# Kernel optimization log

Hardware: AMD Instinct MI355X
Metric: run time of the kernel (lower is better)

## Reference

```python
import jax, jax.numpy as jnp
import numpy as np

B, N, IN_NF, EDGE_NF = 2, 512, 3, 1
DIM, HEADS, DHEAD, DEPTH = 256, 8, 32, 2
INNER = HEADS * DHEAD
SCALE = DHEAD ** -0.5


def _layernorm(x, g, b):
    m = jnp.mean(x, axis=-1, keepdims=True)
    v = jnp.mean((x - m) ** 2, axis=-1, keepdims=True)
    return (x - m) / jnp.sqrt(v + 1e-5) * g + b


def _rotate_half(x):
    x1, x2 = jnp.split(x, 2, axis=-1)
    return jnp.concatenate([-x2, x1], axis=-1)


def _rotary_freqs(n):
    inv_freq = 1.0 / (10000.0 ** (jnp.arange(0, DHEAD, 2, dtype=jnp.float32) / DHEAD))
    f = jnp.einsum('i,j->ij', jnp.arange(n, dtype=jnp.float32), inv_freq)
    return jnp.concatenate([f, f], axis=-1)  # [n, DHEAD]


def _apply_rotary(freqs, t):
    return t * jnp.cos(freqs) + _rotate_half(t) * jnp.sin(freqs)


def _cdist(x):
    # pairwise L2 distances with grad-safe sqrt at zero (matches torch.cdist fwd)
    d2 = jnp.sum((x[:, :, None, :] - x[:, None, :, :]) ** 2, axis=-1)
    safe = jnp.where(d2 > 0.0, d2, 1.0)
    return jnp.where(d2 > 0.0, jnp.sqrt(safe), 0.0)


def setup_inputs():
    key = jax.random.key(0)
    ks = jax.random.split(key, 12)
    w = lambda k, *shape: jax.random.normal(k, shape, dtype=jnp.float32) * 0.02
    return dict(
        x=jax.random.normal(ks[0], (B, N, IN_NF), dtype=jnp.float32),
        t=jax.random.uniform(ks[1], (B, N, 1), dtype=jnp.float32),
        W_enc=w(ks[2], IN_NF + 1, DIM),
        W_dec=w(ks[3], DIM, IN_NF),
        ln_g=jnp.ones((DEPTH, DIM), jnp.float32),
        ln_b=jnp.zeros((DEPTH, DIM), jnp.float32),
        Wq=w(ks[4], DEPTH, DIM, INNER),
        bq=jnp.zeros((DEPTH, INNER), jnp.float32),
        Wkv=w(ks[5], DEPTH, DIM, 2 * INNER),
        bkv=jnp.zeros((DEPTH, 2 * INNER), jnp.float32),
        We=w(ks[6], DEPTH, EDGE_NF, INNER),
        be=jnp.zeros((DEPTH, INNER), jnp.float32),
        Wo=w(ks[7], DEPTH, INNER, DIM),
        bo=jnp.zeros((DEPTH, DIM), jnp.float32),
        Wg=w(ks[8], DEPTH, 3 * DIM, 1),
    )


def _forward(x, t, W_enc, W_dec, ln_g, ln_b, Wq, bq, Wkv, bkv, We, be, Wo, bo, Wg):
    b, n, _ = x.shape
    edges = _cdist(x)[..., None]                         # [B,N,N,1]
    nodes = jnp.concatenate([x, t], axis=-1) @ W_enc     # [B,N,DIM]
    freqs = _rotary_freqs(n)
    for l in range(DEPTH):
        h = _layernorm(nodes, ln_g[l], ln_b[l])          # PreNorm
        q = (h @ Wq[l] + bq[l]).reshape(b, n, HEADS, DHEAD).transpose(0, 2, 1, 3)
        k, v = jnp.split(h @ Wkv[l] + bkv[l], 2, axis=-1)
        k = k.reshape(b, n, HEADS, DHEAD).transpose(0, 2, 1, 3)
        v = v.reshape(b, n, HEADS, DHEAD).transpose(0, 2, 1, 3)
        e = (edges @ We[l] + be[l]).reshape(b, n, n, HEADS, DHEAD)  # [B,i,j,H,D]
        q = _apply_rotary(freqs, q)
        k = _apply_rotary(freqs, k)
        # sim = q . (k_j + e_ij); split to avoid an extra [B,H,N,N,D] materialization
        sim = (jnp.einsum('bhid,bhjd->bhij', q, k)
               + jnp.einsum('bhid,bijhd->bhij', q, e)) * SCALE
        attn = jax.nn.softmax(sim, axis=-1)
        # out = attn . (v_j + e_ij)
        out = (jnp.einsum('bhij,bhjd->bhid', attn, v)
               + jnp.einsum('bhij,bijhd->bhid', attn, e))
        out = out.transpose(0, 2, 1, 3).reshape(b, n, INNER) @ Wo[l] + bo[l]
        # gated residual
        gate = jax.nn.sigmoid(
            jnp.concatenate([out, nodes, out - nodes], axis=-1) @ Wg[l])
        nodes = out * gate + nodes * (1.0 - gate)
    return nodes @ W_dec                                  # [B,N,IN_NF]


def reference(x, t, W_enc, W_dec, ln_g, ln_b, Wq, bq, Wkv, bkv, We, be, Wo, bo, Wg):
    return _forward(x, t, W_enc, W_dec, ln_g, ln_b, Wq, bq, Wkv, bkv, We, be, Wo, bo, Wg)
```

## Files before the change

### kernel.cpp

```cpp
#include <hip/hip_runtime.h>
#include <math.h>

#define B 2
#define N 512
#define DIM 256
#define HEADS 8
#define DHEAD 32
#define INNER 256
#define DEPTH 2
#define SCALE 0.17677669529663687f

__device__ __forceinline__ float block_sum256(float v, float* red4) {
    #pragma unroll
    for (int o = 32; o; o >>= 1) v += __shfl_xor(v, o);
    int tid = threadIdx.x;
    __syncthreads();
    if ((tid & 63) == 0) red4[tid >> 6] = v;
    __syncthreads();
    return red4[0] + red4[1] + red4[2] + red4[3];
}

__global__ void k_pre(const float* __restrict__ x, const float* __restrict__ t,
                      const float* __restrict__ Wenc,
                      const float* __restrict__ ln_g, const float* __restrict__ ln_b,
                      float* __restrict__ nodes, float* __restrict__ hbuf,
                      float* __restrict__ dist,
                      float* __restrict__ ct, float* __restrict__ st) {
    __shared__ float red4[4];
    __shared__ float xs[N * 3];
    int row = blockIdx.x, d = threadIdx.x;
    int b = row >> 9, i = row & (N - 1);

    if (d < 8) {
        int idx = blockIdx.x * 8 + d;
        int ii = idx >> 4, jj = idx & 15;
        float invf = powf(10000.0f, -(float)jj / 16.0f);
        float ang = (float)ii * invf;
        ct[idx] = cosf(ang);
        st[idx] = sinf(ang);
    }

    float x0 = x[row*3+0], x1 = x[row*3+1], x2 = x[row*3+2], tt = t[row];
    float nv = x0*Wenc[d] + x1*Wenc[DIM+d] + x2*Wenc[2*DIM+d] + tt*Wenc[3*DIM+d];
    nodes[row*DIM + d] = nv;
    float mean = block_sum256(nv, red4) * (1.0f/DIM);
    float c = nv - mean;
    float var = block_sum256(c*c, red4) * (1.0f/DIM);
    hbuf[row*DIM + d] = c * (1.0f/sqrtf(var + 1e-5f)) * ln_g[d] + ln_b[d];

    for (int f = d; f < N*3; f += 256) xs[f] = x[b*N*3 + f];
    __syncthreads();
    float xi0 = xs[i*3+0], xi1 = xs[i*3+1], xi2 = xs[i*3+2];
    for (int j = d; j < N; j += 256) {
        float d0 = xi0 - xs[j*3+0], d1 = xi1 - xs[j*3+1], d2 = xi2 - xs[j*3+2];
        float s = d0*d0 + d1*d1 + d2*d2;
        dist[(size_t)row*N + j] = (s > 0.f) ? sqrtf(s) : 0.f;
    }
}

__global__ __launch_bounds__(256, 4)
void k_gemm_qkv(const float* __restrict__ hbuf,
                const float* __restrict__ Wq, const float* __restrict__ bq,
                const float* __restrict__ Wkv, const float* __restrict__ bkv,
                const float* __restrict__ We, const float* __restrict__ be,
                const float* __restrict__ ct, const float* __restrict__ st,
                float* __restrict__ qbuf, float* __restrict__ kbuf, float* __restrict__ vbuf,
                float* __restrict__ qwe, float* __restrict__ qbe, int layer) {
    __shared__ float AT[64][32];
    __shared__ float Bs[64][64];

    int tid = threadIdx.x;
    int mt = blockIdx.x & 31;
    int nt = blockIdx.x >> 5;
    int tx = tid & 15, ty = tid >> 4;
    int n0 = nt * 64;

    const float* Wsrc; int wstride;
    if (n0 < 256) { Wsrc = Wq  + (size_t)layer*256*256 + n0;        wstride = 256; }
    else          { Wsrc = Wkv + (size_t)layer*256*512 + (n0-256);  wstride = 512; }

    float acc[2][4] = {{0,0,0,0},{0,0,0,0}};

    int am = tid & 31, ak = tid >> 5;
    int bn4 = tid & 15, bk = tid >> 4;

    for (int kt = 0; kt < 4; ++kt) {
        int kbase = kt * 64;
        if (kt) __syncthreads();
        {
            const float* src = hbuf + (size_t)(mt*32 + am)*256 + kbase + ak*8;
            float4 a0 = *(const float4*)src;
            float4 a1 = *(const float4*)(src + 4);
            AT[ak*8+0][am]=a0.x; AT[ak*8+1][am]=a0.y; AT[ak*8+2][am]=a0.z; AT[ak*8+3][am]=a0.w;
            AT[ak*8+4][am]=a1.x; AT[ak*8+5][am]=a1.y; AT[ak*8+6][am]=a1.z; AT[ak*8+7][am]=a1.w;
        }
        #pragma unroll
        for (int p = 0; p < 4; ++p) {
            int k = bk + p*16;
            float4 v = *(const float4*)(Wsrc + (size_t)(kbase + k)*wstride + bn4*4);
            *(float4*)&Bs[k][bn4*4] = v;
        }
        __syncthreads();
        #pragma unroll 8
        for (int k = 0; k < 64; ++k) {
            float2 a = *(const float2*)&AT[k][ty*2];
            float4 b = *(const float4*)&Bs[k][tx*4];
            acc[0][0] += a.x*b.x; acc[0][1] += a.x*b.y; acc[0][2] += a.x*b.z; acc[0][3] += a.x*b.w;
            acc[1][0] += a.y*b.x; acc[1][1] += a.y*b.y; acc[1][2] += a.y*b.z; acc[1][3] += a.y*b.w;
        }
    }

    int row = mt*32 + ty*2;
    int n = n0 + tx*4;

    float4 bias4;
    if (n0 < 256) bias4 = *(const float4*)&bq[layer*256 + n];
    else          bias4 = *(const float4*)&bkv[layer*512 + (n - 256)];
    #pragma unroll
    for (int r = 0; r < 2; ++r) {
        acc[r][0] += bias4.x; acc[r][1] += bias4.y; acc[r][2] += bias4.z; acc[r][3] += bias4.w;
    }

    if (n0 >= 512) {
        #pragma unroll
        for (int r = 0; r < 2; ++r) {
            float4 o = make_float4(acc[r][0], acc[r][1], acc[r][2], acc[r][3]);
            *(float4*)&vbuf[(size_t)(row + r)*256 + (n - 512)] = o;
        }
        return;
    }

    float* sh = &Bs[0][0];
    __syncthreads();
    #pragma unroll
    for (int r = 0; r < 2; ++r)
        #pragma unroll
        for (int c = 0; c < 4; ++c)
            sh[(ty*2 + r)*68 + tx*4 + c] = acc[r][c];
    __syncthreads();

    float wep[2] = {0.f, 0.f}, bep[2] = {0.f, 0.f};
    float val[2][4];
    #pragma unroll
    for (int r = 0; r < 2; ++r) {
        int ii = (row + r) & (N-1);
        #pragma unroll
        for (int c = 0; c < 4; ++c) {
            int tc = tx*4 + c;
            int dd = tc & 31, jj = tc & 15;
            float ca = ct[ii*16 + jj], sa = st[ii*16 + jj];
            int ptc = (dd < 16) ? tc + 16 : tc - 16;
            float sgn = (dd < 16) ? -1.f : 1.f;
            float partner = sh[(ty*2 + r)*68 + ptc];
            float rot = acc[r][c]*ca + sgn*partner*sa;
            val[r][c] = rot;
            if (n0 < 256) {
                wep[r] += rot * We[layer*256 + n0 + tc];
                bep[r] += rot * be[layer*256 + n0 + tc];
            }
        }
    }

    float* dst = (n0 < 256) ? qbuf : kbuf;
    int coln = (n0 < 256) ? n : n - 256;
    #pragma unroll
    for (int r = 0; r < 2; ++r) {
        float4 o = make_float4(val[r][0], val[r][1], val[r][2], val[r][3]);
        *(float4*)&dst[(size_t)(row + r)*256 + coln] = o;
    }

    if (n0 < 256) {
        #pragma unroll
        for (int r = 0; r < 2; ++r) {
            wep[r] += __shfl_xor(wep[r], 1); bep[r] += __shfl_xor(bep[r], 1);
            wep[r] += __shfl_xor(wep[r], 2); bep[r] += __shfl_xor(bep[r], 2);
            wep[r] += __shfl_xor(wep[r], 4); bep[r] += __shfl_xor(bep[r], 4);
        }
        if ((tid & 7) == 0) {
            int h = nt*2 + (tx >> 3);
            int bb = row >> 9;
            #pragma unroll
            for (int r = 0; r < 2; ++r) {
                int ii = (row + r) & (N-1);
                qwe[(bb*HEADS + h)*N + ii] = wep[r];
                qbe[(bb*HEADS + h)*N + ii] = bep[r];
            }
        }
    }
}

#define TI 16
__global__ __launch_bounds__(256, 2)
void k_attn(const float* __restrict__ qbuf, const float* __restrict__ kbuf,
            const float* __restrict__ vbuf,
            const float* __restrict__ qwe, const float* __restrict__ qbe,
            const float* __restrict__ dist,
            const float* __restrict__ We, const float* __restrict__ be,
            float* __restrict__ attnout, int layer) {
    __shared__ float Tt[32 * 128];

    int t = threadIdx.x;
    int g = t & 31;
    int r = t >> 5;
    int bid = blockIdx.x;
    int itile = bid & 31;
    int h = (bid >> 5) & (HEADS-1);
    int b = bid >> 8;
    int i0 = itile * TI + r;
    int i1 = i0 + 8;

    int scol = t & 127;
    int d0   = (t >> 7) * 16;

    float q0[32], q1[32];
    {
        const float4* qp0 = (const float4*)(qbuf + (size_t)(b*N + i0) * INNER + h * DHEAD);
        const float4* qp1 = (const float4*)(qbuf + (size_t)(b*N + i1) * INNER + h * DHEAD);
        #pragma unroll
        for (int c = 0; c < 8; ++c) {
            float4 v0 = qp0[c], v1 = qp1[c];
            q0[c*4+0] = v0.x; q0[c*4+1] = v0.y; q0[c*4+2] = v0.z; q0[c*4+3] = v0.w;
            q1[c*4+0] = v1.x; q1[c*4+1] = v1.y; q1[c*4+2] = v1.z; q1[c*4+3] = v1.w;
        }
    }
    float qw0 = qwe[(b*HEADS + h)*N + i0], qb0 = qbe[(b*HEADS + h)*N + i0];
    float qw1 = qwe[(b*HEADS + h)*N + i1], qb1 = qbe[(b*HEADS + h)*N + i1];

    const float* kbase = kbuf + (size_t)b*N*INNER + h*DHEAD;
    const float* vbase = vbuf + (size_t)b*N*INNER + h*DHEAD;
    const float* drow0 = dist + (size_t)(b*N + i0) * N;
    const float* drow1 = dist + (size_t)(b*N + i1) * N;

    float sim0[16], sim1[16];

    #pragma unroll
    for (int jt = 0; jt < 4; ++jt) {
        if (jt) __syncthreads();
        {
            const float* src = kbase + (size_t)(jt*128 + scol) * INNER + d0;
            float4 a0 = *(const float4*)(src + 0);
            float4 a1 = *(const float4*)(src + 4);
            float4 a2 = *(const float4*)(src + 8);
            float4 a3 = *(const float4*)(src + 12);
            Tt[(d0+ 0)*128 + scol] = a0.x; Tt[(d0+ 1)*128 + scol] = a0.y;
            Tt[(d0+ 2)*128 + scol] = a0.z; Tt[(d0+ 3)*128 + scol] = a0.w;
            Tt[(d0+ 4)*128 + scol] = a1.x; Tt[(d0+ 5)*128 + scol] = a1.y;
            Tt[(d0+ 6)*128 + scol] = a1.z; Tt[(d0+ 7)*128 + scol] = a1.w;
            Tt[(d0+ 8)*128 + scol] = a2.x; Tt[(d0+ 9)*128 + scol] = a2.y;
            Tt[(d0+10)*128 + scol] = a2.z; Tt[(d0+11)*128 + scol] = a2.w;
            Tt[(d0+12)*128 + scol] = a3.x; Tt[(d0+13)*128 + scol] = a3.y;
            Tt[(d0+14)*128 + scol] = a3.z; Tt[(d0+15)*128 + scol] = a3.w;
        }
        __syncthreads();
        float4 s0 = make_float4(0.f,0.f,0.f,0.f);
        float4 s1 = make_float4(0.f,0.f,0.f,0.f);
        #pragma unroll
        for (int d = 0; d < 32; ++d) {
            float4 kv = *(const float4*)&Tt[d*128 + g*4];
            float qa = q0[d], qc = q1[d];
            s0.x += qa*kv.x; s0.y += qa*kv.y; s0.z += qa*kv.z; s0.w += qa*kv.w;
            s1.x += qc*kv.x; s1.y += qc*kv.y; s1.z += qc*kv.z; s1.w += qc*kv.w;
        }
        float4 dv0 = *(const float4*)&drow0[jt*128 + g*4];
        float4 dv1 = *(const float4*)&drow1[jt*128 + g*4];
        sim0[jt*4+0] = (s0.x + dv0.x*qw0 + qb0) * SCALE;
        sim0[jt*4+1] = (s0.y + dv0.y*qw0 + qb0) * SCALE;
        sim0[jt*4+2] = (s0.z + dv0.z*qw0 + qb0) * SCALE;
        sim0[jt*4+3] = (s0.w + dv0.w*qw0 + qb0) * SCALE;
        sim1[jt*4+0] = (s1.x + dv1.x*qw1 + qb1) * SCALE;
        sim1[jt*4+1] = (s1.y + dv1.y*qw1 + qb1) * SCALE;
        sim1[jt*4+2] = (s1.z + dv1.z*qw1 + qb1) * SCALE;
        sim1[jt*4+3] = (s1.w + dv1.w*qw1 + qb1) * SCALE;
    }

    float mx0 = -1e30f, mx1 = -1e30f;
    #pragma unroll
    for (int v = 0; v < 16; ++v) { mx0 = fmaxf(mx0, sim0[v]); mx1 = fmaxf(mx1, sim1[v]); }
    #pragma unroll
    for (int o = 1; o <= 16; o <<= 1) {
        mx0 = fmaxf(mx0, __shfl_xor(mx0, o));
        mx1 = fmaxf(mx1, __shfl_xor(mx1, o));
    }

    float ls0 = 0.f, ld0 = 0.f, ls1 = 0.f, ld1 = 0.f;
    #pragma unroll
    for (int jt = 0; jt < 4; ++jt) {
        float4 dv0 = *(const float4*)&drow0[jt*128 + g*4];
        float4 dv1 = *(const float4*)&drow1[jt*128 + g*4];
        float a0[4] = {dv0.x,dv0.y,dv0.z,dv0.w};
        float a1[4] = {dv1.x,dv1.y,dv1.z,dv1.w};
        #pragma unroll
        for (int u = 0; u < 4; ++u) {
            float p0 = __expf(sim0[jt*4+u] - mx0);
            float p1 = __expf(sim1[jt*4+u] - mx1);
            sim0[jt*4+u] = p0; sim1[jt*4+u] = p1;
            ls0 += p0; ld0 += p0 * a0[u];
            ls1 += p1; ld1 += p1 * a1[u];
        }
    }
    #pragma unroll
    for (int o = 1; o <= 16; o <<= 1) {
        ls0 += __shfl_xor(ls0, o); ld0 += __shfl_xor(ld0, o);
        ls1 += __shfl_xor(ls1, o); ld1 += __shfl_xor(ld1, o);
    }

    float acc0[32], acc1[32];
    #pragma unroll
    for (int d = 0; d < 32; ++d) { acc0[d] = 0.f; acc1[d] = 0.f; }

    #pragma unroll
    for (int jt = 0; jt < 4; ++jt) {
        __syncthreads();
        {
            const float* src = vbase + (size_t)(jt*128 + scol) * INNER + d0;
            float4 a0 = *(const float4*)(src + 0);
            float4 a1 = *(const float4*)(src + 4);
            float4 a2 = *(const float4*)(src + 8);
            float4 a3 = *(const float4*)(src + 12);
            Tt[(d0+ 0)*128 + scol] = a0.x; Tt[(d0+ 1)*128 + scol] = a0.y;
            Tt[(d0+ 2)*128 + scol] = a0.z; Tt[(d0+ 3)*128 + scol] = a0.w;
            Tt[(d0+ 4)*128 + scol] = a1.x; Tt[(d0+ 5)*128 + scol] = a1.y;
            Tt[(d0+ 6)*128 + scol] = a1.z; Tt[(d0+ 7)*128 + scol] = a1.w;
            Tt[(d0+ 8)*128 + scol] = a2.x; Tt[(d0+ 9)*128 + scol] = a2.y;
            Tt[(d0+10)*128 + scol] = a2.z; Tt[(d0+11)*128 + scol] = a2.w;
            Tt[(d0+12)*128 + scol] = a3.x; Tt[(d0+13)*128 + scol] = a3.y;
            Tt[(d0+14)*128 + scol] = a3.z; Tt[(d0+15)*128 + scol] = a3.w;
        }
        __syncthreads();
        float p00 = sim0[jt*4+0], p01 = sim0[jt*4+1], p02 = sim0[jt*4+2], p03 = sim0[jt*4+3];
        float p10 = sim1[jt*4+0], p11 = sim1[jt*4+1], p12 = sim1[jt*4+2], p13 = sim1[jt*4+3];
        #pragma unroll
        for (int d = 0; d < 32; ++d) {
            float4 vv = *(const float4*)&Tt[d*128 + g*4];
            acc0[d] += p00*vv.x + p01*vv.y + p02*vv.z + p03*vv.w;
            acc1[d] += p10*vv.x + p11*vv.y + p12*vv.z + p13*vv.w;
        }
    }

    #pragma unroll
    for (int d = 0; d < 32; ++d) {
        #pragma unroll
        for (int o = 1; o <= 16; o <<= 1) {
            acc0[d] += __shfl_xor(acc0[d], o);
            acc1[d] += __shfl_xor(acc1[d], o);
        }
    }

    float il0 = 1.0f / ls0, il1 = 1.0f / ls1;
    float ad0 = ld0 * il0, ad1 = ld1 * il1;
    float o0 = acc0[0], o1 = acc1[0];
    #pragma unroll
    for (int d = 1; d < 32; ++d) if (g == d) { o0 = acc0[d]; o1 = acc1[d]; }
    float wv = We[layer*INNER + h*DHEAD + g];
    float bv = be[layer*INNER + h*DHEAD + g];
    attnout[(size_t)(b*N + i0)*INNER + h*DHEAD + g] = o0*il0 + ad0*wv + bv;
    attnout[(size_t)(b*N + i1)*INNER + h*DHEAD + g] = o1*il1 + ad1*wv + bv;
}

__global__ __launch_bounds__(256, 4)
void k_gemm_o(const float* __restrict__ attnout, const float* __restrict__ Wo,
              const float* __restrict__ bo, float* __restrict__ obuf, int layer) {
    __shared__ float AT[64][32];
    __shared__ float Bs[64][32];
    int tid = threadIdx.x;
    int mt = blockIdx.x & 31, nt = blockIdx.x >> 5;
    int tx = tid & 7, ty = tid >> 3;

    float acc[4] = {0,0,0,0};
    int am = tid & 31, ak = tid >> 5;
    int bn4 = tid & 7, bk = tid >> 3;
    const float* Wsrc = Wo + (size_t)layer*256*256 + nt*32;

    for (int kt = 0; kt < 4; ++kt) {
        int kbase = kt * 64;
        if (kt) __syncthreads();
        {
            const float* src = attnout + (size_t)(mt*32 + am)*256 + kbase + ak*8;
            float4 a0 = *(const float4*)src;
            float4 a1 = *(const float4*)(src + 4);
            AT[ak*8+0][am]=a0.x; AT[ak*8+1][am]=a0.y; AT[ak*8+2][am]=a0.z; AT[ak*8+3][am]=a0.w;
            AT[ak*8+4][am]=a1.x; AT[ak*8+5][am]=a1.y; AT[ak*8+6][am]=a1.z; AT[ak*8+7][am]=a1.w;
        }
        #pragma unroll
        for (int p = 0; p < 2; ++p) {
            int k = bk + p*32;
            *(float4*)&Bs[k][bn4*4] = *(const float4*)(Wsrc + (size_t)(kbase + k)*256 + bn4*4);
        }
        __syncthreads();
        #pragma unroll 8
        for (int k = 0; k < 64; ++k) {
            float a = AT[k][ty];
            float4 b = *(const float4*)&Bs[k][tx*4];
            acc[0] += a*b.x; acc[1] += a*b.y; acc[2] += a*b.z; acc[3] += a*b.w;
        }
    }
    int row = mt*32 + ty, n = nt*32 + tx*4;
    float4 bias = *(const float4*)&bo[layer*256 + n];
    float4 o = make_float4(acc[0]+bias.x, acc[1]+bias.y, acc[2]+bias.z, acc[3]+bias.w);
    *(float4*)&obuf[(size_t)row*256 + n] = o;
}

__global__ void k_gate_ln(const float* __restrict__ obuf, const float* __restrict__ Wg,
                          const float* __restrict__ ln_g, const float* __restrict__ ln_b,
                          const float* __restrict__ Wdec,
                          float* __restrict__ nodes, float* __restrict__ hbuf,
                          float* __restrict__ out, int layer) {
    __shared__ float red4[4];
    int row = blockIdx.x, d = threadIdx.x;
    float o  = obuf[row*DIM + d];
    float nd = nodes[row*DIM + d];
    const float* Wgl = Wg + layer*3*DIM;
    float s = o*Wgl[d] + nd*Wgl[DIM+d] + (o-nd)*Wgl[2*DIM+d];
    float tot = block_sum256(s, red4);
    float gate = 1.0f/(1.0f + __expf(-tot));
    float nn = o*gate + nd*(1.0f - gate);
    nodes[row*DIM + d] = nn;
    if (layer == 0) {
        float mean = block_sum256(nn, red4) * (1.0f/DIM);
        float c = nn - mean;
        float var = block_sum256(c*c, red4) * (1.0f/DIM);
        hbuf[row*DIM + d] = c * (1.0f/sqrtf(var + 1e-5f)) * ln_g[DIM + d] + ln_b[DIM + d];
    } else {
        float s0 = block_sum256(nn * Wdec[d*3+0], red4);
        float s1 = block_sum256(nn * Wdec[d*3+1], red4);
        float s2 = block_sum256(nn * Wdec[d*3+2], red4);
        if (d == 0) { out[row*3+0] = s0; out[row*3+1] = s1; out[row*3+2] = s2; }
    }
}

extern "C" void kernel_launch(void* const* d_in, const int* in_sizes, int n_in,
                              void* d_out, int out_size, void* d_ws, size_t ws_size,
                              hipStream_t stream) {
    const float* x     = (const float*)d_in[0];
    const float* t     = (const float*)d_in[1];
    const float* W_enc = (const float*)d_in[2];
    const float* W_dec = (const float*)d_in[3];
    const float* ln_g  = (const float*)d_in[4];
    const float* ln_b  = (const float*)d_in[5];
    const float* Wq    = (const float*)d_in[6];
    const float* bq    = (const float*)d_in[7];
    const float* Wkv   = (const float*)d_in[8];
    const float* bkv   = (const float*)d_in[9];
    const float* We    = (const float*)d_in[10];
    const float* be    = (const float*)d_in[11];
    const float* Wo    = (const float*)d_in[12];
    const float* bo    = (const float*)d_in[13];
    const float* Wg    = (const float*)d_in[14];
    float* out = (float*)d_out;

    float* ws = (float*)d_ws;
    float* nodes   = ws;
    float* dist    = nodes   + B*N*DIM;
    float* hbuf    = dist    + B*N*N;
    float* qbuf    = hbuf    + B*N*DIM;
    float* kbuf    = qbuf    + B*N*INNER;
    float* vbuf    = kbuf    + B*N*INNER;
    float* qwe     = vbuf    + B*N*INNER;
    float* qbe     = qwe     + B*HEADS*N;
    float* attnout = qbe     + B*HEADS*N;
    float* obuf    = attnout + B*N*INNER;
    float* ct      = obuf    + B*N*DIM;
    float* st      = ct      + N*16;

    k_pre<<<B*N, DIM, 0, stream>>>(x, t, W_enc, ln_g, ln_b, nodes, hbuf, dist, ct, st);
    for (int l = 0; l < DEPTH; ++l) {
        k_gemm_qkv<<<384, 256, 0, stream>>>(hbuf, Wq, bq, Wkv, bkv, We, be, ct, st,
                                            qbuf, kbuf, vbuf, qwe, qbe, l);
        k_attn<<<B*HEADS*(N/TI), 256, 0, stream>>>(qbuf, kbuf, vbuf, qwe, qbe, dist, We, be,
                                                   attnout, l);
        k_gemm_o<<<256, 256, 0, stream>>>(attnout, Wo, bo, obuf, l);
        k_gate_ln<<<B*N, DIM, 0, stream>>>(obuf, Wg, ln_g, ln_b, W_dec, nodes, hbuf, out, l);
    }
}
```

Before: 113.3 us.

## Fuse encoder/gate/layernorm into QKV GEMM and recompute distances inside attention

Removes the separate pre-processing and gate/layernorm kernels. The encoder, or the previous layer's gated residual plus layernorm, is now computed per 32-row tile inside the QKV GEMM prologue and kept in shared memory. Pairwise distances are recomputed from coordinates held in shared memory inside attention instead of being read from a materialized N×N buffer. Rotary sin/cos are also computed inline instead of looked up from tables. This cuts two launches and global traffic, at the cost of every column-tile block repeating the layernorm and gate work. Attention also does extra sqrt work.

```diff
diff --git a/kernel.cpp b/kernel.cpp
--- a/kernel.cpp
+++ b/kernel.cpp
@@ -9,6 +9,7 @@
 #define INNER 256
 #define DEPTH 2
 #define SCALE 0.17677669529663687f
+#define L2INVF 0.8304820237218406f
 
 __device__ __forceinline__ float block_sum256(float v, float* red4) {
     #pragma unroll
@@ -20,93 +21,107 @@
     return red4[0] + red4[1] + red4[2] + red4[3];
 }
 
-__global__ void k_pre(const float* __restrict__ x, const float* __restrict__ t,
-                      const float* __restrict__ Wenc,
-                      const float* __restrict__ ln_g, const float* __restrict__ ln_b,
-                      float* __restrict__ nodes, float* __restrict__ hbuf,
-                      float* __restrict__ dist,
-                      float* __restrict__ ct, float* __restrict__ st) {
-    __shared__ float red4[4];
-    __shared__ float xs[N * 3];
-    int row = blockIdx.x, d = threadIdx.x;
-    int b = row >> 9, i = row & (N - 1);
-
-    if (d < 8) {
-        int idx = blockIdx.x * 8 + d;
-        int ii = idx >> 4, jj = idx & 15;
-        float invf = powf(10000.0f, -(float)jj / 16.0f);
-        float ang = (float)ii * invf;
-        ct[idx] = cosf(ang);
-        st[idx] = sinf(ang);
-    }
-
-    float x0 = x[row*3+0], x1 = x[row*3+1], x2 = x[row*3+2], tt = t[row];
-    float nv = x0*Wenc[d] + x1*Wenc[DIM+d] + x2*Wenc[2*DIM+d] + tt*Wenc[3*DIM+d];
-    nodes[row*DIM + d] = nv;
-    float mean = block_sum256(nv, red4) * (1.0f/DIM);
-    float c = nv - mean;
-    float var = block_sum256(c*c, red4) * (1.0f/DIM);
-    hbuf[row*DIM + d] = c * (1.0f/sqrtf(var + 1e-5f)) * ln_g[d] + ln_b[d];
-
-    for (int f = d; f < N*3; f += 256) xs[f] = x[b*N*3 + f];
-    __syncthreads();
-    float xi0 = xs[i*3+0], xi1 = xs[i*3+1], xi2 = xs[i*3+2];
-    for (int j = d; j < N; j += 256) {
-        float d0 = xi0 - xs[j*3+0], d1 = xi1 - xs[j*3+1], d2 = xi2 - xs[j*3+2];
-        float s = d0*d0 + d1*d1 + d2*d2;
-        dist[(size_t)row*N + j] = (s > 0.f) ? sqrtf(s) : 0.f;
-    }
-}
-
-__global__ __launch_bounds__(256, 4)
-void k_gemm_qkv(const float* __restrict__ hbuf,
-                const float* __restrict__ Wq, const float* __restrict__ bq,
-                const float* __restrict__ Wkv, const float* __restrict__ bkv,
-                const float* __restrict__ We, const float* __restrict__ be,
-                const float* __restrict__ ct, const float* __restrict__ st,
-                float* __restrict__ qbuf, float* __restrict__ kbuf, float* __restrict__ vbuf,
-                float* __restrict__ qwe, float* __restrict__ qbe, int layer) {
-    __shared__ float AT[64][32];
-    __shared__ float Bs[64][64];
+__device__ __forceinline__ float wave_sum(float v) {
+    #pragma unroll
+    for (int o = 32; o; o >>= 1) v += __shfl_xor(v, o);
+    return v;
+}
+
+#define AHS 260
+__global__ __launch_bounds__(256, 3)
+void k_qkv(const float* __restrict__ x, const float* __restrict__ t,
+           const float* __restrict__ Wenc,
+           const float* __restrict__ obuf, const float* __restrict__ nodes,
+           float* __restrict__ nodes2, const float* __restrict__ Wg,
+           const float* __restrict__ ln_g, const float* __restrict__ ln_b,
+           const float* __restrict__ Wq, const float* __restrict__ bq,
+           const float* __restrict__ Wkv, const float* __restrict__ bkv,
+           const float* __restrict__ We, const float* __restrict__ be,
+           float* __restrict__ qbuf, float* __restrict__ kbuf, float* __restrict__ vbuf,
+           float* __restrict__ qwe, float* __restrict__ qbe, int layer) {
+    __shared__ float Ah[32 * AHS];
+    __shared__ float Bs[64 * 64];
 
     int tid = threadIdx.x;
     int mt = blockIdx.x & 31;
     int nt = blockIdx.x >> 5;
+    int n0 = nt * 64;
+
+    {
+        int wv = tid >> 6, lane = tid & 63;
+        int c0 = lane * 4;
+        for (int rr = wv; rr < 32; rr += 4) {
+            int row = mt*32 + rr;
+            float4 v;
+            if (layer == 0) {
+                float x0 = x[row*3+0], x1 = x[row*3+1], x2 = x[row*3+2], tt = t[row];
+                float4 w0 = *(const float4*)&Wenc[c0];
+                float4 w1 = *(const float4*)&Wenc[DIM + c0];
+                float4 w2 = *(const float4*)&Wenc[2*DIM + c0];
+                float4 w3 = *(const float4*)&Wenc[3*DIM + c0];
+                v.x = x0*w0.x + x1*w1.x + x2*w2.x + tt*w3.x;
+                v.y = x0*w0.y + x1*w1.y + x2*w2.y + tt*w3.y;
+                v.z = x0*w0.z + x1*w1.z + x2*w2.z + tt*w3.z;
+                v.w = x0*w0.w + x1*w1.w + x2*w2.w + tt*w3.w;
+                if (nt == 0) *(float4*)&nodes2[(size_t)row*DIM + c0] = v;
+            } else {
+                float4 o4 = *(const float4*)&obuf[(size_t)row*DIM + c0];
+                float4 nd = *(const float4*)&nodes[(size_t)row*DIM + c0];
+                const float* Wgl = Wg;
+                float4 g1 = *(const float4*)&Wgl[c0];
+                float4 g2 = *(const float4*)&Wgl[DIM + c0];
+                float4 g3 = *(const float4*)&Wgl[2*DIM + c0];
+                float sp = o4.x*g1.x + nd.x*g2.x + (o4.x-nd.x)*g3.x
+                         + o4.y*g1.y + nd.y*g2.y + (o4.y-nd.y)*g3.y
+                         + o4.z*g1.z + nd.z*g2.z + (o4.z-nd.z)*g3.z
+                         + o4.w*g1.w + nd.w*g2.w + (o4.w-nd.w)*g3.w;
+                sp = wave_sum(sp);
+                float gate = 1.0f/(1.0f + __expf(-sp));
+                v.x = o4.x*gate + nd.x*(1.f-gate);
+                v.y = o4.y*gate + nd.y*(1.f-gate);
+                v.z = o4.z*gate + nd.z*(1.f-gate);
+                v.w = o4.w*gate + nd.w*(1.f-gate);
+                if (nt == 0) *(float4*)&nodes2[(size_t)row*DIM + c0] = v;
+            }
+            float mean = wave_sum(v.x + v.y + v.z + v.w) * (1.0f/DIM);
+            float4 cc = make_float4(v.x-mean, v.y-mean, v.z-mean, v.w-mean);
+            float vs = wave_sum(cc.x*cc.x + cc.y*cc.y + cc.z*cc.z + cc.w*cc.w);
+            float rs = 1.0f/sqrtf(vs*(1.0f/DIM) + 1e-5f);
+            float4 lg = *(const float4*)&ln_g[layer*DIM + c0];
+            float4 lb = *(const float4*)&ln_b[layer*DIM + c0];
+            Ah[rr*AHS + c0+0] = cc.x*rs*lg.x + lb.x;
+            Ah[rr*AHS + c0+1] = cc.y*rs*lg.y + lb.y;
+            Ah[rr*AHS + c0+2] = cc.z*rs*lg.z + lb.z;
+            Ah[rr*AHS + c0+3] = cc.w*rs*lg.w + lb.w;
+        }
+    }
+    __syncthreads();
+
     int tx = tid & 15, ty = tid >> 4;
-    int n0 = nt * 64;
-
     const float* Wsrc; int wstride;
     if (n0 < 256) { Wsrc = Wq  + (size_t)layer*256*256 + n0;        wstride = 256; }
     else          { Wsrc = Wkv + (size_t)layer*256*512 + (n0-256);  wstride = 512; }
 
     float acc[2][4] = {{0,0,0,0},{0,0,0,0}};
-
-    int am = tid & 31, ak = tid >> 5;
     int bn4 = tid & 15, bk = tid >> 4;
 
     for (int kt = 0; kt < 4; ++kt) {
         int kbase = kt * 64;
         if (kt) __syncthreads();
-        {
-            const float* src = hbuf + (size_t)(mt*32 + am)*256 + kbase + ak*8;
-            float4 a0 = *(const float4*)src;
-            float4 a1 = *(const float4*)(src + 4);
-            AT[ak*8+0][am]=a0.x; AT[ak*8+1][am]=a0.y; AT[ak*8+2][am]=a0.z; AT[ak*8+3][am]=a0.w;
-            AT[ak*8+4][am]=a1.x; AT[ak*8+5][am]=a1.y; AT[ak*8+6][am]=a1.z; AT[ak*8+7][am]=a1.w;
-        }
         #pragma unroll
         for (int p = 0; p < 4; ++p) {
             int k = bk + p*16;
             float4 v = *(const float4*)(Wsrc + (size_t)(kbase + k)*wstride + bn4*4);
-            *(float4*)&Bs[k][bn4*4] = v;
+            *(float4*)&Bs[k*64 + bn4*4] = v;
         }
         __syncthreads();
         #pragma unroll 8
         for (int k = 0; k < 64; ++k) {
-            float2 a = *(const float2*)&AT[k][ty*2];
-            float4 b = *(const float4*)&Bs[k][tx*4];
-            acc[0][0] += a.x*b.x; acc[0][1] += a.x*b.y; acc[0][2] += a.x*b.z; acc[0][3] += a.x*b.w;
-            acc[1][0] += a.y*b.x; acc[1][1] += a.y*b.y; acc[1][2] += a.y*b.z; acc[1][3] += a.y*b.w;
+            float ax = Ah[(ty*2+0)*AHS + kbase + k];
+            float ay = Ah[(ty*2+1)*AHS + kbase + k];
+            float4 b = *(const float4*)&Bs[k*64 + tx*4];
+            acc[0][0] += ax*b.x; acc[0][1] += ax*b.y; acc[0][2] += ax*b.z; acc[0][3] += ax*b.w;
+            acc[1][0] += ay*b.x; acc[1][1] += ay*b.y; acc[1][2] += ay*b.z; acc[1][3] += ay*b.w;
         }
     }
 
@@ -130,7 +145,7 @@
         return;
     }
 
-    float* sh = &Bs[0][0];
+    float* sh = Bs;
     __syncthreads();
     #pragma unroll
     for (int r = 0; r < 2; ++r)
@@ -139,20 +154,31 @@
             sh[(ty*2 + r)*68 + tx*4 + c] = acc[r][c];
     __syncthreads();
 
+    float ca_[2][4], sa_[2][4];
+    #pragma unroll
+    for (int r = 0; r < 2; ++r) {
+        int ii = (row + r) & (N-1);
+        #pragma unroll
+        for (int c = 0; c < 4; ++c) {
+            int jj = (tx*4 + c) & 15;
+            float invf = exp2f(-(float)jj * L2INVF);
+            float ang = (float)ii * invf;
+            sincosf(ang, &sa_[r][c], &ca_[r][c]);
+        }
+    }
+
     float wep[2] = {0.f, 0.f}, bep[2] = {0.f, 0.f};
     float val[2][4];
     #pragma unroll
     for (int r = 0; r < 2; ++r) {
-        int ii = (row + r) & (N-1);
         #pragma unroll
         for (int c = 0; c < 4; ++c) {
             int tc = tx*4 + c;
-            int dd = tc & 31, jj = tc & 15;
-            float ca = ct[ii*16 + jj], sa = st[ii*16 + jj];
+            int dd = tc & 31;
             int ptc = (dd < 16) ? tc + 16 : tc - 16;
             float sgn = (dd < 16) ? -1.f : 1.f;
             float partner = sh[(ty*2 + r)*68 + ptc];
-            float rot = acc[r][c]*ca + sgn*partner*sa;
+            float rot = acc[r][c]*ca_[r][c] + sgn*partner*sa_[r][c];
             val[r][c] = rot;
             if (n0 < 256) {
                 wep[r] += rot * We[layer*256 + n0 + tc];
@@ -191,13 +217,14 @@
 
 #define TI 16
 __global__ __launch_bounds__(256, 2)
-void k_attn(const float* __restrict__ qbuf, const float* __restrict__ kbuf,
+void k_attn(const float* __restrict__ x,
+            const float* __restrict__ qbuf, const float* __restrict__ kbuf,
             const float* __restrict__ vbuf,
             const float* __restrict__ qwe, const float* __restrict__ qbe,
-            const float* __restrict__ dist,
             const float* __restrict__ We, const float* __restrict__ be,
             float* __restrict__ attnout, int layer) {
     __shared__ float Tt[32 * 128];
+    __shared__ float xs[N * 3];
 
     int t = threadIdx.x;
     int g = t & 31;
@@ -212,6 +239,11 @@
     int scol = t & 127;
     int d0   = (t >> 7) * 16;
 
+    for (int f = t; f < N*3; f += 256) xs[f] = x[b*N*3 + f];
+    __syncthreads();
+    float xa0 = xs[i0*3+0], xa1 = xs[i0*3+1], xa2 = xs[i0*3+2];
+    float xb0 = xs[i1*3+0], xb1 = xs[i1*3+1], xb2 = xs[i1*3+2];
+
     float q0[32], q1[32];
     {
         const float4* qp0 = (const float4*)(qbuf + (size_t)(b*N + i0) * INNER + h * DHEAD);
@@ -228,8 +260,6 @@
 
     const float* kbase = kbuf + (size_t)b*N*INNER + h*DHEAD;
     const float* vbase = vbuf + (size_t)b*N*INNER + h*DHEAD;
-    const float* drow0 = dist + (size_t)(b*N + i0) * N;
-    const float* drow1 = dist + (size_t)(b*N + i1) * N;
 
     float sim0[16], sim1[16];
 
@@ -261,16 +291,20 @@
             s0.x += qa*kv.x; s0.y += qa*kv.y; s0.z += qa*kv.z; s0.w += qa*kv.w;
             s1.x += qc*kv.x; s1.y += qc*kv.y; s1.z += qc*kv.z; s1.w += qc*kv.w;
         }
-        float4 dv0 = *(const float4*)&drow0[jt*128 + g*4];
-        float4 dv1 = *(const float4*)&drow1[jt*128 + g*4];
-        sim0[jt*4+0] = (s0.x + dv0.x*qw0 + qb0) * SCALE;
-        sim0[jt*4+1] = (s0.y + dv0.y*qw0 + qb0) * SCALE;
-        sim0[jt*4+2] = (s0.z + dv0.z*qw0 + qb0) * SCALE;
-        sim0[jt*4+3] = (s0.w + dv0.w*qw0 + qb0) * SCALE;
-        sim1[jt*4+0] = (s1.x + dv1.x*qw1 + qb1) * SCALE;
-        sim1[jt*4+1] = (s1.y + dv1.y*qw1 + qb1) * SCALE;
-        sim1[jt*4+2] = (s1.z + dv1.z*qw1 + qb1) * SCALE;
-        sim1[jt*4+3] = (s1.w + dv1.w*qw1 + qb1) * SCALE;
+        #pragma unroll
+        for (int u = 0; u < 4; ++u) {
+            int j = jt*128 + g*4 + u;
+            float e0 = xa0 - xs[j*3+0], e1 = xa1 - xs[j*3+1], e2 = xa2 - xs[j*3+2];
+            float ss = e0*e0 + e1*e1 + e2*e2;
+            float dv0 = (ss > 0.f) ? sqrtf(ss) : 0.f;
+            float f0 = xb0 - xs[j*3+0], f1 = xb1 - xs[j*3+1], f2 = xb2 - xs[j*3+2];
+            float tt2 = f0*f0 + f1*f1 + f2*f2;
+            float dv1 = (tt2 > 0.f) ? sqrtf(tt2) : 0.f;
+            float sv0 = (u==0) ? s0.x : (u==1) ? s0.y : (u==2) ? s0.z : s0.w;
+            float sv1 = (u==0) ? s1.x : (u==1) ? s1.y : (u==2) ? s1.z : s1.w;
+            sim0[jt*4+u] = (sv0 + dv0*qw0 + qb0) * SCALE;
+            sim1[jt*4+u] = (sv1 + dv1*qw1 + qb1) * SCALE;
+        }
     }
 
     float mx0 = -1e30f, mx1 = -1e30f;
@@ -285,17 +319,20 @@
     float ls0 = 0.f, ld0 = 0.f, ls1 = 0.f, ld1 = 0.f;
     #pragma unroll
     for (int jt = 0; jt < 4; ++jt) {
-        float4 dv0 = *(const float4*)&drow0[jt*128 + g*4];
-        float4 dv1 = *(const float4*)&drow1[jt*128 + g*4];
-        float a0[4] = {dv0.x,dv0.y,dv0.z,dv0.w};
-        float a1[4] = {dv1.x,dv1.y,dv1.z,dv1.w};
         #pragma unroll
         for (int u = 0; u < 4; ++u) {
+            int j = jt*128 + g*4 + u;
+            float e0 = xa0 - xs[j*3+0], e1 = xa1 - xs[j*3+1], e2 = xa2 - xs[j*3+2];
+            float ss = e0*e0 + e1*e1 + e2*e2;
+            float dv0 = (ss > 0.f) ? sqrtf(ss) : 0.f;
+            float f0 = xb0 - xs[j*3+0], f1 = xb1 - xs[j*3+1], f2 = xb2 - xs[j*3+2];
+            float tt2 = f0*f0 + f1*f1 + f2*f2;
+            float dv1 = (tt2 > 0.f) ? sqrtf(tt2) : 0.f;
             float p0 = __expf(sim0[jt*4+u] - mx0);
             float p1 = __expf(sim1[jt*4+u] - mx1);
             sim0[jt*4+u] = p0; sim1[jt*4+u] = p1;
-            ls0 += p0; ld0 += p0 * a0[u];
-            ls1 += p1; ld1 += p1 * a1[u];
+            ls0 += p0; ld0 += p0 * dv0;
+            ls1 += p1; ld1 += p1 * dv1;
         }
     }
     #pragma unroll
@@ -400,32 +437,22 @@
     *(float4*)&obuf[(size_t)row*256 + n] = o;
 }
 
-__global__ void k_gate_ln(const float* __restrict__ obuf, const float* __restrict__ Wg,
-                          const float* __restrict__ ln_g, const float* __restrict__ ln_b,
-                          const float* __restrict__ Wdec,
-                          float* __restrict__ nodes, float* __restrict__ hbuf,
-                          float* __restrict__ out, int layer) {
+__global__ void k_gate_dec(const float* __restrict__ obuf, const float* __restrict__ Wg,
+                           const float* __restrict__ nodes2, const float* __restrict__ Wdec,
+                           float* __restrict__ out) {
     __shared__ float red4[4];
     int row = blockIdx.x, d = threadIdx.x;
     float o  = obuf[row*DIM + d];
-    float nd = nodes[row*DIM + d];
-    const float* Wgl = Wg + layer*3*DIM;
+    float nd = nodes2[row*DIM + d];
+    const float* Wgl = Wg + 3*DIM;
     float s = o*Wgl[d] + nd*Wgl[DIM+d] + (o-nd)*Wgl[2*DIM+d];
     float tot = block_sum256(s, red4);
     float gate = 1.0f/(1.0f + __expf(-tot));
     float nn = o*gate + nd*(1.0f - gate);
-    nodes[row*DIM + d] = nn;
-    if (layer == 0) {
-        float mean = block_sum256(nn, red4) * (1.0f/DIM);
-        float c = nn - mean;
-        float var = block_sum256(c*c, red4) * (1.0f/DIM);
-        hbuf[row*DIM + d] = c * (1.0f/sqrtf(var + 1e-5f)) * ln_g[DIM + d] + ln_b[DIM + d];
-    } else {
-        float s0 = block_sum256(nn * Wdec[d*3+0], red4);
-        float s1 = block_sum256(nn * Wdec[d*3+1], red4);
-        float s2 = block_sum256(nn * Wdec[d*3+2], red4);
-        if (d == 0) { out[row*3+0] = s0; out[row*3+1] = s1; out[row*3+2] = s2; }
-    }
+    float s0 = block_sum256(nn * Wdec[d*3+0], red4);
+    float s1 = block_sum256(nn * Wdec[d*3+1], red4);
+    float s2 = block_sum256(nn * Wdec[d*3+2], red4);
+    if (d == 0) { out[row*3+0] = s0; out[row*3+1] = s1; out[row*3+2] = s2; }
 }
 
 extern "C" void kernel_launch(void* const* d_in, const int* in_sizes, int n_in,
@@ -450,25 +477,28 @@
 
     float* ws = (float*)d_ws;
     float* nodes   = ws;
-    float* dist    = nodes   + B*N*DIM;
-    float* hbuf    = dist    + B*N*N;
-    float* qbuf    = hbuf    + B*N*DIM;
+    float* nodes2  = nodes   + B*N*DIM;
+    float* qbuf    = nodes2  + B*N*DIM;
     float* kbuf    = qbuf    + B*N*INNER;
     float* vbuf    = kbuf    + B*N*INNER;
     float* qwe     = vbuf    + B*N*INNER;
     float* qbe     = qwe     + B*HEADS*N;
     float* attnout = qbe     + B*HEADS*N;
     float* obuf    = attnout + B*N*INNER;
-    float* ct      = obuf    + B*N*DIM;
-    float* st      = ct      + N*16;
-
-    k_pre<<<B*N, DIM, 0, stream>>>(x, t, W_enc, ln_g, ln_b, nodes, hbuf, dist, ct, st);
-    for (int l = 0; l < DEPTH; ++l) {
-        k_gemm_qkv<<<384, 256, 0, stream>>>(hbuf, Wq, bq, Wkv, bkv, We, be, ct, st,
-                                            qbuf, kbuf, vbuf, qwe, qbe, l);
-        k_attn<<<B*HEADS*(N/TI), 256, 0, stream>>>(qbuf, kbuf, vbuf, qwe, qbe, dist, We, be,
-                                                   attnout, l);
-        k_gemm_o<<<256, 256, 0, stream>>>(attnout, Wo, bo, obuf, l);
-        k_gate_ln<<<B*N, DIM, 0, stream>>>(obuf, Wg, ln_g, ln_b, W_dec, nodes, hbuf, out, l);
-    }
-}
+
+    k_qkv<<<384, 256, 0, stream>>>(x, t, W_enc, obuf, nodes, nodes, Wg, ln_g, ln_b,
+                                   Wq, bq, Wkv, bkv, We, be,
+                                   qbuf, kbuf, vbuf, qwe, qbe, 0);
+    k_attn<<<B*HEADS*(N/TI), 256, 0, stream>>>(x, qbuf, kbuf, vbuf, qwe, qbe, We, be,
+                                               attnout, 0);
+    k_gemm_o<<<256, 256, 0, stream>>>(attnout, Wo, bo, obuf, 0);
+
+    k_qkv<<<384, 256, 0, stream>>>(x, t, W_enc, obuf, nodes, nodes2, Wg, ln_g, ln_b,
+                                   Wq, bq, Wkv, bkv, We, be,
+                                   qbuf, kbuf, vbuf, qwe, qbe, 1);
+    k_attn<<<B*HEADS*(N/TI), 256, 0, stream>>>(x, qbuf, kbuf, vbuf, qwe, qbe, We, be,
+                                               attnout, 1);
+    k_gemm_o<<<256, 256, 0, stream>>>(attnout, Wo, bo, obuf, 1);
+
+    k_gate_dec<<<B*N, 256, 0, stream>>>(obuf, Wg, nodes2, W_dec, out);
+}
```

After: 122.5 us. +8.1%, slower.
